# Performance work log

Measured on AMD Instinct MI355X. Metric: run time of the kernel, lower is better.

Reference implementation:

```python
import jax, jax.numpy as jnp
import numpy as np

BN_EPS = 1e-5

def conv3d(x, w, b):
    # standard 3D conv, stride 1, pad 1, NCDHW
    out = jax.lax.conv_general_dilated(x, w, (1, 1, 1), ((1, 1), (1, 1), (1, 1)),
                                       dimension_numbers=('NCDHW', 'OIDHW', 'NCDHW'))
    return out + b[None, :, None, None, None]

def batchnorm(x, gamma, beta):
    # training-mode BN over (B, D, H, W) per channel
    mu = x.mean(axis=(0, 2, 3, 4), keepdims=True)
    var = x.var(axis=(0, 2, 3, 4), keepdims=True)
    g = gamma[None, :, None, None, None]
    b = beta[None, :, None, None, None]
    return g * (x - mu) * jax.lax.rsqrt(var + BN_EPS) + b

def deform_conv3d(x, offset, weight, cpg):
    # x: [B,C,D,H,W]; offset: [B, G*27*3, D,H,W] with layout [B,G,27,(d,h,w),D,H,W]
    # weight: [C_out, C_in, 3,3,3]; kernel 3, stride 1, pad 1 -> same spatial size
    B, C, D, H, W = x.shape
    G = C // cpg
    off = offset.reshape(B, G, 27, 3, D, H, W)
    k = jnp.arange(27)
    kd = (k // 9 - 1).astype(x.dtype).reshape(1, 1, 27, 1, 1, 1)
    kh = ((k // 3) % 3 - 1).astype(x.dtype).reshape(1, 1, 27, 1, 1, 1)
    kw = (k % 3 - 1).astype(x.dtype).reshape(1, 1, 27, 1, 1, 1)
    gd = jnp.arange(D, dtype=x.dtype).reshape(1, 1, 1, D, 1, 1)
    gh = jnp.arange(H, dtype=x.dtype).reshape(1, 1, 1, 1, H, 1)
    gw = jnp.arange(W, dtype=x.dtype).reshape(1, 1, 1, 1, 1, W)
    # fractional sampling positions per (batch, group, tap, voxel): [B,G,27,D,H,W]
    pd = gd + kd + off[:, :, :, 0]
    ph = gh + kh + off[:, :, :, 1]
    pw = gw + kw + off[:, :, :, 2]
    d0 = jnp.floor(pd); h0 = jnp.floor(ph); w0 = jnp.floor(pw)
    fd = pd - d0; fh = ph - h0; fw = pw - w0
    d0i = d0.astype(jnp.int32); h0i = h0.astype(jnp.int32); w0i = w0.astype(jnp.int32)
    xg = x.reshape(B, G, cpg, D * H * W)
    N = 27 * D * H * W
    acc = jnp.zeros((B, G, cpg, 27, D, H, W), x.dtype)
    for dd in (0, 1):
        for hh in (0, 1):
            for ww in (0, 1):
                di = d0i + dd; hi = h0i + hh; wi = w0i + ww
                wgt = ((fd if dd else 1.0 - fd) * (fh if hh else 1.0 - fh)
                       * (fw if ww else 1.0 - fw))
                valid = ((di >= 0) & (di < D) & (hi >= 0) & (hi < H)
                         & (wi >= 0) & (wi < W))  # zero padding outside
                dic = jnp.clip(di, 0, D - 1)
                hic = jnp.clip(hi, 0, H - 1)
                wic = jnp.clip(wi, 0, W - 1)
                idx = ((dic * H + hic) * W + wic).reshape(B, G, 1, N)
                vals = jnp.take_along_axis(xg, jnp.broadcast_to(idx, (B, G, cpg, N)), axis=3)
                vals = vals.reshape(B, G, cpg, 27, D, H, W)
                acc = acc + (wgt * valid)[:, :, None] * vals
    wr = weight.reshape(weight.shape[0], G, cpg, 27)
    return jnp.einsum('bgckdhw,ogck->bodhw', acc, wr)

def setup_inputs() -> dict:
    key = jax.random.key(0)
    ks = jax.random.split(key, 8)
    B, C, D, H, W = 2, 64, 8, 32, 32
    cpg = 8
    Coff = (C // cpg) * 3 * 27  # 648
    fan = 1.0 / np.sqrt(C * 27)
    x = jax.random.normal(ks[0], (B, C, D, H, W), jnp.float32)
    w_off1 = jax.random.normal(ks[1], (Coff, C, 3, 3, 3), jnp.float32) * 0.01
    b_off1 = jnp.zeros((Coff,), jnp.float32)
    w1 = jax.random.normal(ks[2], (C, C, 3, 3, 3), jnp.float32) * fan
    g1 = jnp.ones((C,), jnp.float32)
    be1 = jnp.zeros((C,), jnp.float32)
    w_off2 = jax.random.normal(ks[3], (Coff, C, 3, 3, 3), jnp.float32) * 0.01
    b_off2 = jnp.zeros((Coff,), jnp.float32)
    w2 = jax.random.normal(ks[4], (C, C, 3, 3, 3), jnp.float32) * fan
    g2 = jnp.ones((C,), jnp.float32)
    be2 = jnp.zeros((C,), jnp.float32)
    return {'x': x, 'w_off1': w_off1, 'b_off1': b_off1, 'w1': w1, 'g1': g1,
            'be1': be1, 'w_off2': w_off2, 'b_off2': b_off2, 'w2': w2,
            'g2': g2, 'be2': be2, 'cpg': cpg}

def reference(x, w_off1, b_off1, w1, g1, be1, w_off2, b_off2, w2, g2, be2, cpg):
    off1 = conv3d(x, w_off1, b_off1)
    out = deform_conv3d(x, off1, w1, cpg)
    out = jax.nn.relu(batchnorm(out, g1, be1))
    off2 = conv3d(x, w_off2, b_off2)  # note: offsets computed from x, as in source
    out = deform_conv3d(out, off2, w2, cpg)
    out = batchnorm(out, g2, be2) + x
    out = jax.nn.relu(out)
    return (out, off1, off2)
```

## Files before the change

### kernel.cpp

```cpp
#include <hip/hip_runtime.h>
#include <stdint.h>

typedef unsigned short u16;
typedef __attribute__((ext_vector_type(8))) short bf16x8;
typedef __attribute__((ext_vector_type(4))) float f32x4;

#define DEV static __device__ __forceinline__

#define BB    2
#define CC    64
#define DDD   8
#define HHH   32
#define WWW   32
#define DHW   8192
#define MTOT  16384
#define GG    8
#define KTOT  1728
#define NOFF  1296
#define NOFFP 1408
#define COFF  648

#define OFF1_ELEM (BB*CC*DHW)
#define OFF2_ELEM (OFF1_ELEM + BB*COFF*DHW)

#define XCL_OFF   0ull
#define YCL_OFF   2097152ull
#define WOFF_OFF  4194304ull
#define W1_OFF    9060352ull
#define W2_OFF    9281536ull
#define C1_OFF    9502720ull
#define C2_OFF    13697024ull
#define ST1_OFF   17891328ull
#define ST2_OFF   17891840ull
#define ZPG_OFF   17892352ull
#define PART_OFF  17892608ull

DEV float bf2f(u16 u){ union { uint32_t i; float f; } v; v.i = ((uint32_t)u) << 16; return v.f; }
DEV u16 f2bf(float f){ union { float f; uint32_t i; } v; v.f = f;
  uint32_t r = v.i + 0x7fffu + ((v.i >> 16) & 1u); return (u16)(r >> 16); }

DEV void gld16(const void* g, void* l){
  __builtin_amdgcn_global_load_lds((const __attribute__((address_space(1))) void*)g,
                                   (__attribute__((address_space(3))) void*)l, 16, 0, 0);
}

__global__ void k_zero(uint32_t* z){ z[threadIdx.x] = 0u; }

__global__ void k_prep_xcl(const float* __restrict__ x, u16* __restrict__ xcl){
  int idx = blockIdx.x * 256 + threadIdx.x;
  if (idx >= BB*CC*DHW) return;
  int p = idx & (DHW - 1);
  int c = (idx >> 13) & 63;
  int b = idx >> 19;
  xcl[(size_t)(b * DHW + p) * CC + c] = f2bf(x[idx]);
}

__global__ void k_prep_woff(const float* __restrict__ wa, const float* __restrict__ wb,
                            u16* __restrict__ wo){
  int idx = blockIdx.x * 256 + threadIdx.x;
  if (idx >= NOFFP * KTOT) return;
  int k = idx % KTOT, n = idx / KTOT;
  int tap = k >> 6, cin = k & 63;
  float v = 0.f;
  if (n < NOFF) {
    const float* w = (n < COFF) ? wa : wb;
    int nn = (n < COFF) ? n : n - COFF;
    v = w[(size_t)nn * KTOT + cin * 27 + tap];
  }
  wo[idx] = f2bf(v);
}

__global__ void k_prep_w(const float* __restrict__ w, u16* __restrict__ wb){
  int idx = blockIdx.x * 256 + threadIdx.x;
  if (idx >= CC * KTOT) return;
  int k = idx % KTOT, n = idx / KTOT;
  int tap = k >> 6, cin = k & 63;
  wb[idx] = f2bf(w[(size_t)n * KTOT + cin * 27 + tap]);
}

__global__ __launch_bounds__(512) void k_gemm_off(
    const u16* __restrict__ xcl, const u16* __restrict__ woff,
    const float* __restrict__ boff1, const float* __restrict__ boff2,
    float* __restrict__ dout, const u16* __restrict__ zpg)
{
  __shared__ u16 Al[256 * 64];
  __shared__ u16 Bl[128 * 64];
  const int tid = threadIdx.x;
  const int wv = tid >> 6, lane = tid & 63;
  const int m0 = blockIdx.x * 256;
  const int n0 = blockIdx.y * 128;
  const int lr = lane >> 3, lc = lane & 7;
  const int lcs = (lc ^ lr) << 3;
  const int b  = m0 >> 13;
  const int p0 = m0 & (DHW - 1);
  int ad[4], ah[4], aw[4];
  #pragma unroll
  for (int i = 0; i < 4; ++i) {
    int p = p0 + wv * 32 + i * 8 + lr;
    ad[i] = p >> 10; ah[i] = (p >> 5) & 31; aw[i] = p & 31;
  }
  const size_t xb = (size_t)b * DHW * CC;

  f32x4 acc[4][4] = {};
  const int wm = wv >> 1, wn = wv & 1;
  const int r16 = lane & 15, q = lane >> 4;
  const int rs = r16 & 7;

  for (int t = 0; t < 27; ++t) {
    int kd = t / 9 - 1, kh = (t / 3) % 3 - 1, kw = t % 3 - 1;
    #pragma unroll
    for (int i = 0; i < 4; ++i) {
      int d2 = ad[i] + kd, h2 = ah[i] + kh, w2 = aw[i] + kw;
      bool ok = ((unsigned)d2 < DDD) & ((unsigned)h2 < HHH) & ((unsigned)w2 < WWW);
      const u16* src = ok ? (xcl + xb + (size_t)((d2 << 10) + (h2 << 5) + w2) * CC + lcs)
                          : zpg;
      gld16(src, &Al[(wv * 32 + i * 8) * 64]);
    }
    #pragma unroll
    for (int i = 0; i < 2; ++i) {
      int r = wv * 16 + i * 8 + lr;
      const u16* src = woff + (size_t)(n0 + r) * KTOT + t * 64 + lcs;
      gld16(src, &Bl[(wv * 16 + i * 8) * 64]);
    }
    __syncthreads();
    #pragma unroll
    for (int kk = 0; kk < 2; ++kk) {
      const int cs = ((kk * 4 + q) ^ rs) << 3;
      bf16x8 af[4], bfr[4];
      #pragma unroll
      for (int i = 0; i < 4; ++i)
        af[i] = *(const bf16x8*)&Al[(wm * 64 + i * 16 + r16) * 64 + cs];
      #pragma unroll
      for (int j = 0; j < 4; ++j)
        bfr[j] = *(const bf16x8*)&Bl[(wn * 64 + j * 16 + r16) * 64 + cs];
      #pragma unroll
      for (int i = 0; i < 4; ++i)
        #pragma unroll
        for (int j = 0; j < 4; ++j)
          acc[i][j] = __builtin_amdgcn_mfma_f32_16x16x32_bf16(af[i], bfr[j], acc[i][j], 0, 0, 0);
    }
    __syncthreads();
  }

  float biasj[4]; int ncj[4];
  #pragma unroll
  for (int j = 0; j < 4; ++j) {
    int nc = n0 + wn * 64 + j * 16 + r16;
    ncj[j] = nc;
    biasj[j] = (nc < NOFF) ? ((nc < COFF) ? boff1[nc] : boff2[nc - COFF]) : 0.f;
  }
  #pragma unroll
  for (int i = 0; i < 4; ++i) {
    int mrow = m0 + wm * 64 + i * 16 + q * 4;
    int bb = mrow >> 13, p = mrow & (DHW - 1);
    #pragma unroll
    for (int j = 0; j < 4; ++j) {
      int nc = ncj[j];
      if (nc < NOFF) {
        int ch = (nc < COFF) ? nc : nc - COFF;
        size_t base = (nc < COFF) ? (size_t)OFF1_ELEM : (size_t)OFF2_ELEM;
        f32x4 v = acc[i][j] + biasj[j];
        *(f32x4*)(dout + base + ((size_t)(bb * COFF + ch)) * DHW + p) = v;
      }
    }
  }
}

__global__ __launch_bounds__(512) void k_deform(
    const u16* __restrict__ src, const float* __restrict__ offs,
    const u16* __restrict__ wB, float* __restrict__ cdst,
    const u16* __restrict__ zpg)
{
  __shared__ u16 Al[2 * 32 * 64];
  __shared__ u16 Bl[2 * 64 * 64];
  const int tid = threadIdx.x;
  const int wv = tid >> 6, lane = tid & 63;
  const int mrow0 = blockIdx.x * 32;
  const int b  = mrow0 >> 13;
  const int p0 = mrow0 & (DHW - 1);

  const int pl = tid & 31;
  const int g  = (tid >> 5) & 7;
  const int th = tid >> 8;
  const int p  = p0 + pl;
  const int d = p >> 10, h = (p >> 5) & 31, w = p & 31;
  const u16* sb = src + (size_t)b * DHW * CC + g * 8;
  const size_t obase = ((size_t)(b * COFF + g * 81)) * DHW + p;
  u16* awp = &Al[th * 2048 + pl * 64 + ((g ^ (pl & 7)) << 3)];

  const int brow = (tid >> 3) & 63;
  const int bch  = tid & 7;
  const int bcs  = ((bch ^ (brow & 7)) << 3);

  f32x4 acc = {};
  const int wm = wv >> 2, wn = wv & 3;
  const int r16 = lane & 15, q = lane >> 4;
  const int rs = r16 & 7;

  for (int ph = 0; ph < 14; ++ph) {
    #pragma unroll
    for (int i = 0; i < 2; ++i) {
      int tb = 2 * ph + i;
      const u16* s = (tb < 27) ? (wB + (size_t)brow * KTOT + tb * 64 + bcs) : zpg;
      gld16(s, &Bl[(i * 512 + wv * 64) * 8]);
    }
    {
      int t = 2 * ph + th;
      float a8[8] = {0.f,0.f,0.f,0.f,0.f,0.f,0.f,0.f};
      if (t < 27) {
        int kd = t / 9 - 1, kh = (t / 3) % 3 - 1, kw = t % 3 - 1;
        size_t ob = obase + (size_t)(t * 3) * DHW;
        float pd = (float)(d + kd) + offs[ob];
        float phh = (float)(h + kh) + offs[ob + DHW];
        float pw = (float)(w + kw) + offs[ob + 2 * DHW];
        float fd0 = floorf(pd), fh0 = floorf(phh), fw0 = floorf(pw);
        float fd = pd - fd0, fh = phh - fh0, fw = pw - fw0;
        int d0 = (int)fd0, h0 = (int)fh0, w0 = (int)fw0;
        #pragma unroll
        for (int dd = 0; dd < 2; ++dd) {
          float wd = dd ? fd : 1.f - fd;
          int di = d0 + dd;
          #pragma unroll
          for (int hh = 0; hh < 2; ++hh) {
            float wh = hh ? fh : 1.f - fh;
            int hi = h0 + hh;
            #pragma unroll
            for (int ww = 0; ww < 2; ++ww) {
              int wi = w0 + ww;
              if (((unsigned)di < DDD) && ((unsigned)hi < HHH) && ((unsigned)wi < WWW)) {
                float wgt = wd * wh * (ww ? fw : 1.f - fw);
                bf16x8 v = *(const bf16x8*)(sb + (size_t)((di << 10) + (hi << 5) + wi) * CC);
                #pragma unroll
                for (int c = 0; c < 8; ++c) a8[c] += wgt * bf2f((u16)v[c]);
              }
            }
          }
        }
      }
      union { bf16x8 v; u16 u[8]; } o;
      #pragma unroll
      for (int c = 0; c < 8; ++c) o.u[c] = f2bf(a8[c]);
      *(bf16x8*)awp = o.v;
    }
    __syncthreads();
    #pragma unroll
    for (int tt = 0; tt < 2; ++tt) {
      #pragma unroll
      for (int kk = 0; kk < 2; ++kk) {
        const int cs = ((kk * 4 + q) ^ rs) << 3;
        bf16x8 af = *(const bf16x8*)&Al[tt * 2048 + (wm * 16 + r16) * 64 + cs];
        bf16x8 bf_ = *(const bf16x8*)&Bl[tt * 4096 + (wn * 16 + r16) * 64 + cs];
        acc = __builtin_amdgcn_mfma_f32_16x16x32_bf16(af, bf_, acc, 0, 0, 0);
      }
    }
    __syncthreads();
  }

  {
    int nc = wn * 16 + r16;
    int mr = mrow0 + wm * 16 + q * 4;
    #pragma unroll
    for (int r = 0; r < 4; ++r)
      cdst[(size_t)(mr + r) * CC + nc] = acc[r];
  }
}

__global__ void k_bnpart(const float* __restrict__ c, float* __restrict__ part)
{
  int k = blockIdx.x, tid = threadIdx.x;
  int ch = tid & 63, sub = tid >> 6;
  float s = 0.f, s2 = 0.f;
  for (int mm = sub; mm < 64; mm += 4) {
    float v = c[(size_t)(k * 64 + mm) * CC + ch];
    s += v; s2 += v * v;
  }
  __shared__ float sh[4][128];
  sh[sub][ch] = s; sh[sub][64 + ch] = s2;
  __syncthreads();
  if (tid < 128)
    part[(size_t)k * 128 + tid] = sh[0][tid] + sh[1][tid] + sh[2][tid] + sh[3][tid];
}

__global__ void k_bnfin(const float* __restrict__ part, const float* __restrict__ gamma,
                        const float* __restrict__ beta, float* __restrict__ stats)
{
  int n = threadIdx.x;
  float S = 0.f, S2 = 0.f;
  for (int k = 0; k < 256; ++k) {
    S  += part[(size_t)k * 128 + n];
    S2 += part[(size_t)k * 128 + 64 + n];
  }
  float mu = S / (float)MTOT;
  float var = S2 / (float)MTOT - mu * mu;
  float sc = gamma[n] / sqrtf(var + 1e-5f);
  stats[n] = sc;
  stats[64 + n] = beta[n] - mu * sc;
}

__global__ void k_apply1(const float* __restrict__ c1, const float* __restrict__ st,
                         u16* __restrict__ ycl)
{
  int idx = blockIdx.x * 256 + threadIdx.x;
  if (idx >= MTOT * CC) return;
  int n = idx & 63;
  float v = st[n] * c1[idx] + st[64 + n];
  ycl[idx] = f2bf(fmaxf(v, 0.f));
}

__global__ void k_apply2(const float* __restrict__ c2, const float* __restrict__ st,
                         const float* __restrict__ x, float* __restrict__ out)
{
  int idx = blockIdx.x * 256 + threadIdx.x;
  if (idx >= BB * CC * DHW) return;
  int p = idx & (DHW - 1);
  int n = (idx >> 13) & 63;
  int b = idx >> 19;
  float v = st[n] * c2[(size_t)(b * DHW + p) * CC + n] + st[64 + n] + x[idx];
  out[idx] = fmaxf(v, 0.f);
}

extern "C" void kernel_launch(void* const* d_in, const int* in_sizes, int n_in,
                              void* d_out, int out_size, void* d_ws, size_t ws_size,
                              hipStream_t stream)
{
  (void)in_sizes; (void)n_in; (void)out_size; (void)ws_size;
  const float* x      = (const float*)d_in[0];
  const float* w_off1 = (const float*)d_in[1];
  const float* b_off1 = (const float*)d_in[2];
  const float* w1     = (const float*)d_in[3];
  const float* g1     = (const float*)d_in[4];
  const float* be1    = (const float*)d_in[5];
  const float* w_off2 = (const float*)d_in[6];
  const float* b_off2 = (const float*)d_in[7];
  const float* w2     = (const float*)d_in[8];
  const float* g2     = (const float*)d_in[9];
  const float* be2    = (const float*)d_in[10];

  char* ws = (char*)d_ws;
  u16*   xcl  = (u16*)(ws + XCL_OFF);
  u16*   ycl  = (u16*)(ws + YCL_OFF);
  u16*   woff = (u16*)(ws + WOFF_OFF);
  u16*   w1b  = (u16*)(ws + W1_OFF);
  u16*   w2b  = (u16*)(ws + W2_OFF);
  float* c1   = (float*)(ws + C1_OFF);
  float* c2   = (float*)(ws + C2_OFF);
  float* st1  = (float*)(ws + ST1_OFF);
  float* st2  = (float*)(ws + ST2_OFF);
  u16*   zpg  = (u16*)(ws + ZPG_OFF);
  float* part = (float*)(ws + PART_OFF);
  float* out  = (float*)d_out;

  k_zero<<<1, 64, 0, stream>>>((uint32_t*)zpg);
  k_prep_xcl<<<(BB*CC*DHW) / 256, 256, 0, stream>>>(x, xcl);
  k_prep_woff<<<(NOFFP * KTOT + 255) / 256, 256, 0, stream>>>(w_off1, w_off2, woff);
  k_prep_w<<<(CC * KTOT + 255) / 256, 256, 0, stream>>>(w1, w1b);
  k_prep_w<<<(CC * KTOT + 255) / 256, 256, 0, stream>>>(w2, w2b);

  k_gemm_off<<<dim3(MTOT / 256, NOFFP / 128), 512, 0, stream>>>(
      xcl, woff, b_off1, b_off2, out, zpg);

  k_deform<<<MTOT / 32, 512, 0, stream>>>(xcl, out + OFF1_ELEM, w1b, c1, zpg);
  k_bnpart<<<256, 256, 0, stream>>>(c1, part);
  k_bnfin<<<1, 64, 0, stream>>>(part, g1, be1, st1);
  k_apply1<<<(MTOT * CC) / 256, 256, 0, stream>>>(c1, st1, ycl);

  k_deform<<<MTOT / 32, 512, 0, stream>>>(ycl, out + OFF2_ELEM, w2b, c2, zpg);
  k_bnpart<<<256, 256, 0, stream>>>(c2, part);
  k_bnfin<<<1, 64, 0, stream>>>(part, g2, be2, st2);
  k_apply2<<<(BB*CC*DHW) / 256, 256, 0, stream>>>(c2, st2, x, out);
}
```

Measured before the change: 278.4 us.

## Fuse prep kernels, shrink gemm and deform tiles, skip padded offset columns

Merges the zero-fill and the four weight/input conversion kernels into one launch. The offset GEMM moves to 128x128 tiles with 256 threads, and skips MFMAs for the padded N columns beyond the real offset channel count. The deform kernel moves to 16-row tiles with 256 threads, doubling the block count so more blocks are resident. The aim is to cut launch overhead, wasted padding compute and underutilisation, at the cost of more B-tile reloads per output row.

```diff
diff --git a/kernel.cpp b/kernel.cpp
--- a/kernel.cpp
+++ b/kernel.cpp
@@ -44,50 +44,61 @@
                                    (__attribute__((address_space(3))) void*)l, 16, 0, 0);
 }
 
-__global__ void k_zero(uint32_t* z){ z[threadIdx.x] = 0u; }
-
-__global__ void k_prep_xcl(const float* __restrict__ x, u16* __restrict__ xcl){
+#define PRE0 (BB*CC*DHW)
+#define PRE1 (PRE0 + NOFFP*KTOT)
+#define PRE2 (PRE1 + CC*KTOT)
+#define PRE3 (PRE2 + CC*KTOT)
+#define PRETOT (PRE3 + 128)
+
+__global__ void k_prep(const float* __restrict__ x,
+                       const float* __restrict__ wo1, const float* __restrict__ wo2,
+                       const float* __restrict__ w1, const float* __restrict__ w2,
+                       u16* __restrict__ xcl, u16* __restrict__ woff,
+                       u16* __restrict__ w1b, u16* __restrict__ w2b,
+                       u16* __restrict__ zpg)
+{
   int idx = blockIdx.x * 256 + threadIdx.x;
-  if (idx >= BB*CC*DHW) return;
-  int p = idx & (DHW - 1);
-  int c = (idx >> 13) & 63;
-  int b = idx >> 19;
-  xcl[(size_t)(b * DHW + p) * CC + c] = f2bf(x[idx]);
-}
-
-__global__ void k_prep_woff(const float* __restrict__ wa, const float* __restrict__ wb,
-                            u16* __restrict__ wo){
-  int idx = blockIdx.x * 256 + threadIdx.x;
-  if (idx >= NOFFP * KTOT) return;
-  int k = idx % KTOT, n = idx / KTOT;
-  int tap = k >> 6, cin = k & 63;
-  float v = 0.f;
-  if (n < NOFF) {
-    const float* w = (n < COFF) ? wa : wb;
-    int nn = (n < COFF) ? n : n - COFF;
-    v = w[(size_t)nn * KTOT + cin * 27 + tap];
-  }
-  wo[idx] = f2bf(v);
-}
-
-__global__ void k_prep_w(const float* __restrict__ w, u16* __restrict__ wb){
-  int idx = blockIdx.x * 256 + threadIdx.x;
-  if (idx >= CC * KTOT) return;
-  int k = idx % KTOT, n = idx / KTOT;
-  int tap = k >> 6, cin = k & 63;
-  wb[idx] = f2bf(w[(size_t)n * KTOT + cin * 27 + tap]);
-}
-
-__global__ __launch_bounds__(512) void k_gemm_off(
+  if (idx < PRE0) {
+    int p = idx & (DHW - 1);
+    int c = (idx >> 13) & 63;
+    int b = idx >> 19;
+    xcl[(size_t)(b * DHW + p) * CC + c] = f2bf(x[idx]);
+  } else if (idx < PRE1) {
+    int j = idx - PRE0;
+    int k = j % KTOT, n = j / KTOT;
+    int tap = k >> 6, cin = k & 63;
+    float v = 0.f;
+    if (n < NOFF) {
+      const float* w = (n < COFF) ? wo1 : wo2;
+      int nn = (n < COFF) ? n : n - COFF;
+      v = w[(size_t)nn * KTOT + cin * 27 + tap];
+    }
+    woff[j] = f2bf(v);
+  } else if (idx < PRE2) {
+    int j = idx - PRE1;
+    int k = j % KTOT, n = j / KTOT;
+    int tap = k >> 6, cin = k & 63;
+    w1b[j] = f2bf(w1[(size_t)n * KTOT + cin * 27 + tap]);
+  } else if (idx < PRE3) {
+    int j = idx - PRE2;
+    int k = j % KTOT, n = j / KTOT;
+    int tap = k >> 6, cin = k & 63;
+    w2b[j] = f2bf(w2[(size_t)n * KTOT + cin * 27 + tap]);
+  } else if (idx < PRETOT) {
+    zpg[idx - PRE3] = 0;
+  }
+}
+
+__global__ __launch_bounds__(256) void k_gemm_off(
     const u16* __restrict__ xcl, const u16* __restrict__ woff,
     const float* __restrict__ boff1, const float* __restrict__ boff2,
     float* __restrict__ dout, const u16* __restrict__ zpg)
 {
-  __shared__ u16 Al[256 * 64];
+  __shared__ u16 Al[128 * 64];
   __shared__ u16 Bl[128 * 64];
   const int tid = threadIdx.x;
   const int wv = tid >> 6, lane = tid & 63;
-  const int m0 = blockIdx.x * 256;
+  const int m0 = blockIdx.x * 128;
   const int n0 = blockIdx.y * 128;
   const int lr = lane >> 3, lc = lane & 7;
   const int lcs = (lc ^ lr) << 3;
@@ -105,6 +116,8 @@
   const int wm = wv >> 1, wn = wv & 1;
   const int r16 = lane & 15, q = lane >> 4;
   const int rs = r16 & 7;
+  const int nbase = n0 + wn * 64;
+  const int jlim = (nbase >= NOFF) ? 0 : ((NOFF - nbase >= 64) ? 4 : ((NOFF - nbase + 15) >> 4));
 
   for (int t = 0; t < 27; ++t) {
     int kd = t / 9 - 1, kh = (t / 3) % 3 - 1, kw = t % 3 - 1;
@@ -117,27 +130,28 @@
       gld16(src, &Al[(wv * 32 + i * 8) * 64]);
     }
     #pragma unroll
-    for (int i = 0; i < 2; ++i) {
-      int r = wv * 16 + i * 8 + lr;
+    for (int i = 0; i < 4; ++i) {
+      int r = wv * 32 + i * 8 + lr;
       const u16* src = woff + (size_t)(n0 + r) * KTOT + t * 64 + lcs;
-      gld16(src, &Bl[(wv * 16 + i * 8) * 64]);
+      gld16(src, &Bl[(wv * 32 + i * 8) * 64]);
     }
     __syncthreads();
     #pragma unroll
     for (int kk = 0; kk < 2; ++kk) {
       const int cs = ((kk * 4 + q) ^ rs) << 3;
-      bf16x8 af[4], bfr[4];
+      bf16x8 af[4];
       #pragma unroll
       for (int i = 0; i < 4; ++i)
         af[i] = *(const bf16x8*)&Al[(wm * 64 + i * 16 + r16) * 64 + cs];
       #pragma unroll
-      for (int j = 0; j < 4; ++j)
-        bfr[j] = *(const bf16x8*)&Bl[(wn * 64 + j * 16 + r16) * 64 + cs];
-      #pragma unroll
-      for (int i = 0; i < 4; ++i)
-        #pragma unroll
-        for (int j = 0; j < 4; ++j)
-          acc[i][j] = __builtin_amdgcn_mfma_f32_16x16x32_bf16(af[i], bfr[j], acc[i][j], 0, 0, 0);
+      for (int j = 0; j < 4; ++j) {
+        if (j < jlim) {
+          bf16x8 bfr = *(const bf16x8*)&Bl[(wn * 64 + j * 16 + r16) * 64 + cs];
+          #pragma unroll
+          for (int i = 0; i < 4; ++i)
+            acc[i][j] = __builtin_amdgcn_mfma_f32_16x16x32_bf16(af[i], bfr, acc[i][j], 0, 0, 0);
+        }
+      }
     }
     __syncthreads();
   }
@@ -166,43 +180,42 @@
   }
 }
 
-__global__ __launch_bounds__(512) void k_deform(
+__global__ __launch_bounds__(256) void k_deform(
     const u16* __restrict__ src, const float* __restrict__ offs,
     const u16* __restrict__ wB, float* __restrict__ cdst,
     const u16* __restrict__ zpg)
 {
-  __shared__ u16 Al[2 * 32 * 64];
+  __shared__ u16 Al[2 * 16 * 64];
   __shared__ u16 Bl[2 * 64 * 64];
   const int tid = threadIdx.x;
   const int wv = tid >> 6, lane = tid & 63;
-  const int mrow0 = blockIdx.x * 32;
+  const int mrow0 = blockIdx.x * 16;
   const int b  = mrow0 >> 13;
   const int p0 = mrow0 & (DHW - 1);
 
-  const int pl = tid & 31;
-  const int g  = (tid >> 5) & 7;
-  const int th = tid >> 8;
+  const int pl = tid & 15;
+  const int g  = (tid >> 4) & 7;
+  const int th = tid >> 7;
   const int p  = p0 + pl;
   const int d = p >> 10, h = (p >> 5) & 31, w = p & 31;
   const u16* sb = src + (size_t)b * DHW * CC + g * 8;
   const size_t obase = ((size_t)(b * COFF + g * 81)) * DHW + p;
-  u16* awp = &Al[th * 2048 + pl * 64 + ((g ^ (pl & 7)) << 3)];
-
-  const int brow = (tid >> 3) & 63;
-  const int bch  = tid & 7;
-  const int bcs  = ((bch ^ (brow & 7)) << 3);
+  u16* awp = &Al[th * 1024 + pl * 64 + ((g ^ (pl & 7)) << 3)];
+
+  const int lr = lane >> 3, lc = lane & 7;
+  const int lcs = (lc ^ lr) << 3;
 
   f32x4 acc = {};
-  const int wm = wv >> 2, wn = wv & 3;
   const int r16 = lane & 15, q = lane >> 4;
   const int rs = r16 & 7;
 
   for (int ph = 0; ph < 14; ++ph) {
     #pragma unroll
-    for (int i = 0; i < 2; ++i) {
-      int tb = 2 * ph + i;
-      const u16* s = (tb < 27) ? (wB + (size_t)brow * KTOT + tb * 64 + bcs) : zpg;
-      gld16(s, &Bl[(i * 512 + wv * 64) * 8]);
+    for (int i = 0; i < 4; ++i) {
+      int tb = 2 * ph + (i >> 1);
+      int row = (i & 1) * 32 + wv * 8 + lr;
+      const u16* s = (tb < 27) ? (wB + (size_t)row * KTOT + tb * 64 + lcs) : zpg;
+      gld16(s, &Bl[(i >> 1) * 4096 + (((i & 1) * 32 + wv * 8) * 64)]);
     }
     {
       int t = 2 * ph + th;
@@ -248,8 +261,8 @@
       #pragma unroll
       for (int kk = 0; kk < 2; ++kk) {
         const int cs = ((kk * 4 + q) ^ rs) << 3;
-        bf16x8 af = *(const bf16x8*)&Al[tt * 2048 + (wm * 16 + r16) * 64 + cs];
-        bf16x8 bf_ = *(const bf16x8*)&Bl[tt * 4096 + (wn * 16 + r16) * 64 + cs];
+        bf16x8 af = *(const bf16x8*)&Al[tt * 1024 + r16 * 64 + cs];
+        bf16x8 bf_ = *(const bf16x8*)&Bl[tt * 4096 + (wv * 16 + r16) * 64 + cs];
         acc = __builtin_amdgcn_mfma_f32_16x16x32_bf16(af, bf_, acc, 0, 0, 0);
       }
     }
@@ -257,8 +270,8 @@
   }
 
   {
-    int nc = wn * 16 + r16;
-    int mr = mrow0 + wm * 16 + q * 4;
+    int nc = wv * 16 + r16;
+    int mr = mrow0 + q * 4;
     #pragma unroll
     for (int r = 0; r < 4; ++r)
       cdst[(size_t)(mr + r) * CC + nc] = acc[r];
@@ -350,21 +363,18 @@
   float* part = (float*)(ws + PART_OFF);
   float* out  = (float*)d_out;
 
-  k_zero<<<1, 64, 0, stream>>>((uint32_t*)zpg);
-  k_prep_xcl<<<(BB*CC*DHW) / 256, 256, 0, stream>>>(x, xcl);
-  k_prep_woff<<<(NOFFP * KTOT + 255) / 256, 256, 0, stream>>>(w_off1, w_off2, woff);
-  k_prep_w<<<(CC * KTOT + 255) / 256, 256, 0, stream>>>(w1, w1b);
-  k_prep_w<<<(CC * KTOT + 255) / 256, 256, 0, stream>>>(w2, w2b);
-
-  k_gemm_off<<<dim3(MTOT / 256, NOFFP / 128), 512, 0, stream>>>(
+  k_prep<<<(PRETOT + 255) / 256, 256, 0, stream>>>(
+      x, w_off1, w_off2, w1, w2, xcl, woff, w1b, w2b, zpg);
+
+  k_gemm_off<<<dim3(MTOT / 128, NOFFP / 128), 256, 0, stream>>>(
       xcl, woff, b_off1, b_off2, out, zpg);
 
-  k_deform<<<MTOT / 32, 512, 0, stream>>>(xcl, out + OFF1_ELEM, w1b, c1, zpg);
+  k_deform<<<MTOT / 16, 256, 0, stream>>>(xcl, out + OFF1_ELEM, w1b, c1, zpg);
   k_bnpart<<<256, 256, 0, stream>>>(c1, part);
   k_bnfin<<<1, 64, 0, stream>>>(part, g1, be1, st1);
   k_apply1<<<(MTOT * CC) / 256, 256, 0, stream>>>(c1, st1, ycl);
 
-  k_deform<<<MTOT / 32, 512, 0, stream>>>(ycl, out + OFF2_ELEM, w2b, c2, zpg);
+  k_deform<<<MTOT / 16, 256, 0, stream>>>(ycl, out + OFF2_ELEM, w2b, c2, zpg);
   k_bnpart<<<256, 256, 0, stream>>>(c2, part);
   k_bnfin<<<1, 64, 0, stream>>>(part, g2, be2, st2);
   k_apply2<<<(BB*CC*DHW) / 256, 256, 0, stream>>>(c2, st2, x, out);
```

Result: faster. 259.9 us (-6.6%).
